# Kernel tuning notes

Measured on AMD Instinct MI355X. Metric: run time of the kernel, lower is better.

Reference implementation:

```python
import jax, jax.numpy as jnp
import numpy as np

NEG = float(-2**32 + 1)  # huge negative used by the original sign-based masking
EPS = 1e-8
NUM_BLOCKS = 3
NUM_HEADS = 1


def _mha(xq, xk, xv, Wq, bq, Wk, bk, Wv, bv):
    # manual QKV with ReLU, as in the torch module
    Q = jax.nn.relu(xq @ Wq + bq)   # [B, Lq, D]
    K = jax.nn.relu(xk @ Wk + bk)   # [B, Lk, D]
    V = jax.nn.relu(xv @ Wv + bv)
    B, Lq, D = Q.shape
    Lk = K.shape[1]
    dh = D // NUM_HEADS
    Qh = Q.reshape(B, Lq, NUM_HEADS, dh)
    Kh = K.reshape(B, Lk, NUM_HEADS, dh)
    Vh = V.reshape(B, Lk, NUM_HEADS, dh)
    scores = jnp.einsum('bqhd,bkhd->bhqk', Qh, Kh) / jnp.sqrt(jnp.float32(dh))
    # sign-based key padding mask (rows whose embedding-sum is exactly 0)
    key_mask0 = (jnp.sign(jnp.abs(jnp.sum(xk, axis=-1))) == 0.0).astype(scores.dtype)  # [B, Lk]
    cond = key_mask0[:, None, None, :]
    scores = NEG * cond + scores * (1.0 - cond)
    attn = jax.nn.softmax(scores, axis=-1)
    # post-softmax query mask
    qmask = jnp.sign(jnp.abs(jnp.sum(xq, axis=-1)))  # [B, Lq]
    attn = attn * qmask[:, None, :, None]
    out = jnp.einsum('bhqk,bkhd->bqhd', attn, Vh).reshape(B, Lq, D)
    return out + xq  # residual; note: the torch mha never applies its layernorm


def _layernorm(x, g, b):
    mu = jnp.mean(x, axis=-1, keepdims=True)
    var = jnp.mean(jnp.square(x - mu), axis=-1, keepdims=True)
    return (x - mu) / jnp.sqrt(var + EPS) * g + b


def _ffn(x, W1, b1, W2, b2, g, bln):
    h = jax.nn.relu(x @ W1 + b1) @ W2 + b2
    return _layernorm(h, g, bln) + x


def setup_inputs() -> dict:
    key = jax.random.key(0)
    ks = jax.random.split(key, 9)
    B, L, V, D, NB = 4096, 50, 50000, 200, NUM_BLOCKS
    tokens = jax.random.randint(ks[0], (B, L), 0, V)
    emb = jax.random.normal(ks[1], (V, D), dtype=jnp.float32) * 0.1
    emb = emb.at[0].set(0.0)  # padding token row -> triggers sign masks
    s = 1.0 / np.sqrt(D)
    Wq = jax.random.normal(ks[2], (NB, D, D), dtype=jnp.float32) * s
    Wk = jax.random.normal(ks[3], (NB, D, D), dtype=jnp.float32) * s
    Wv = jax.random.normal(ks[4], (NB, D, D), dtype=jnp.float32) * s
    W1 = jax.random.normal(ks[5], (NB, D, D), dtype=jnp.float32) * s
    W2 = jax.random.normal(ks[6], (NB, D, D), dtype=jnp.float32) * s
    z = jnp.zeros((NB, D), dtype=jnp.float32)
    return dict(tokens=tokens, emb=emb,
                Wq=Wq, bq=z, Wk=Wk, bk=z, Wv=Wv, bv=z,
                W1=W1, b1=z, W2=W2, b2=z,
                ln_g=jnp.ones((NB, D), dtype=jnp.float32), ln_b=z)


def reference(tokens, emb, Wq, bq, Wk, bk, Wv, bv, W1, b1, W2, b2, ln_g, ln_b):
    x = emb[tokens]  # [B, L, D]
    for i in range(NUM_BLOCKS):
        x = _mha(x, x, x, Wq[i], bq[i], Wk[i], bk[i], Wv[i], bv[i])
        x = _ffn(x, W1[i], b1[i], W2[i], b2[i], ln_g[i], ln_b[i])
    return x
```

## Files before the change

### kernel.cpp

```cpp
#include <hip/hip_runtime.h>
#include <hip/hip_bf16.h>
#include <math.h>

#define LQ 50
#define DD 200
#define NBLK 3
#define NT 1024
#define NW 16

#define KT 7
#define NTL 14
#define MAT_U (KT * NTL * 128)

#define APS 408
#define VTS 72
#define PS  136
#define SS  66

#define NEGC (-4294967295.0f)
#define SCALE 0.07071067811865475f

typedef __attribute__((ext_vector_type(4))) float f32x4;
typedef __attribute__((ext_vector_type(8))) short s16x8;

__device__ __forceinline__ unsigned short bf16_rne(float x) {
  unsigned u = __float_as_uint(x);
  unsigned r = u + 0x7FFF + ((u >> 16) & 1);
  return (unsigned short)(r >> 16);
}
__device__ __forceinline__ float bf16_f(unsigned short h) {
  return __uint_as_float((unsigned)h << 16);
}

__device__ __forceinline__ void splitf(float x, short& h, short& l) {
  __hip_bfloat16 bh = __float2bfloat16(x);
  float hf = __bfloat162float(bh);
  __hip_bfloat16 bl = __float2bfloat16(x - hf);
  h = (short)__builtin_bit_cast(unsigned short, bh);
  l = (short)__builtin_bit_cast(unsigned short, bl);
}
__device__ __forceinline__ unsigned short bfbits(float x) {
  __hip_bfloat16 bh = __float2bfloat16(x);
  return __builtin_bit_cast(unsigned short, bh);
}
__device__ __forceinline__ float joinf(short h, short l) {
  return __bfloat162float(__builtin_bit_cast(__hip_bfloat16, (unsigned short)h)) +
         __bfloat162float(__builtin_bit_cast(__hip_bfloat16, (unsigned short)l));
}

__device__ __forceinline__ float wave_sum(float v) {
  #pragma unroll
  for (int off = 32; off > 0; off >>= 1) v += __shfl_xor(v, off, 64);
  return v;
}
__device__ __forceinline__ float wave_max(float v) {
  #pragma unroll
  for (int off = 32; off > 0; off >>= 1) v = fmaxf(v, __shfl_xor(v, off, 64));
  return v;
}

__global__ __launch_bounds__(64)
void swizzle_w(const float* __restrict__ Wq, const float* __restrict__ Wk,
               const float* __restrict__ Wv, const float* __restrict__ W1,
               const float* __restrict__ W2, unsigned short* __restrict__ wbuf)
{
  int t = blockIdx.x;
  int nt = t % NTL; t /= NTL;
  int kt = t % KT;  t /= KT;
  int mat = t;
  int layer = mat / 5, which = mat % 5;
  const float* W;
  switch (which) {
    case 0: W = Wq; break;
    case 1: W = Wk; break;
    case 2: W = Wv; break;
    case 3: W = W1; break;
    default: W = W2; break;
  }
  W += (size_t)layer * DD * DD;

  const int l = threadIdx.x;
  const int g = l >> 4, c = l & 15;
  const int n = nt * 16 + c;
  s16x8 vh, vl;
  #pragma unroll
  for (int j = 0; j < 8; ++j) {
    int k = kt * 32 + g * 8 + j;
    float w = (k < DD && n < DD) ? W[k * DD + n] : 0.0f;
    unsigned short h = bf16_rne(w);
    unsigned short lo = bf16_rne(w - bf16_f(h));
    vh[j] = (short)h;
    vl[j] = (short)lo;
  }
  size_t base = ((size_t)(mat * KT * NTL + kt * NTL + nt) * 2) * 512 + l * 8;
  *(s16x8*)(wbuf + base)       = vh;
  *(s16x8*)(wbuf + base + 512) = vl;
}

template <int MODE>
__device__ __forceinline__ void big_matmul(
    const short* __restrict__ srcp, const s16x8* __restrict__ wt,
    const float* __restrict__ bias, short* __restrict__ dstp,
    float* __restrict__ dstf, int wv, int lane)
{
  if (wv >= 13) return;
  const int g = lane >> 4, c = lane & 15;
  const int n1 = wv;

  const short* arow[4];
  #pragma unroll
  for (int m = 0; m < 4; ++m) {
    int r = m * 16 + c;
    if (r >= LQ) r = 0;
    arow[m] = srcp + r * APS;
  }

  f32x4 acc0[4];
  #pragma unroll
  for (int m = 0; m < 4; ++m) acc0[m] = (f32x4)0.f;

  #pragma unroll 1
  for (int kt = 0; kt < KT; ++kt) {
    const s16x8* p1 = wt + ((size_t)kt * NTL + n1) * 128 + lane;
    s16x8 b1h = p1[0], b1l = p1[64];
    const int ch = kt * 4 + g;
    const bool ok = (ch < 25);
    #pragma unroll
    for (int m = 0; m < 4; ++m) {
      s16x8 ah = (s16x8)0, al = (s16x8)0;
      if (ok) {
        const short* ap = arow[m] + ch * 16;
        ah = *(const s16x8*)ap;
        al = *(const s16x8*)(ap + 8);
      }
      if (MODE == 0) {
        acc0[m] = __builtin_amdgcn_mfma_f32_16x16x32_bf16(b1h, ah, acc0[m], 0, 0, 0);
        acc0[m] = __builtin_amdgcn_mfma_f32_16x16x32_bf16(b1h, al, acc0[m], 0, 0, 0);
        acc0[m] = __builtin_amdgcn_mfma_f32_16x16x32_bf16(b1l, ah, acc0[m], 0, 0, 0);
      } else {
        acc0[m] = __builtin_amdgcn_mfma_f32_16x16x32_bf16(ah, b1h, acc0[m], 0, 0, 0);
        acc0[m] = __builtin_amdgcn_mfma_f32_16x16x32_bf16(al, b1h, acc0[m], 0, 0, 0);
        acc0[m] = __builtin_amdgcn_mfma_f32_16x16x32_bf16(ah, b1l, acc0[m], 0, 0, 0);
      }
    }
  }

  if (MODE == 0) {
    const int nb = n1 * 16 + g * 4;
    if (nb + 3 < DD) {
      float4 bv = *(const float4*)(bias + nb);
      #pragma unroll
      for (int m = 0; m < 4; ++m) {
        const int r = m * 16 + c;
        if (r < LQ) {
          const f32x4 ac = acc0[m];
          float v0 = fmaxf(ac[0] + bv.x, 0.f);
          float v1 = fmaxf(ac[1] + bv.y, 0.f);
          float v2 = fmaxf(ac[2] + bv.z, 0.f);
          float v3 = fmaxf(ac[3] + bv.w, 0.f);
          short h0, l0, h1, l1, h2, l2, h3, l3;
          splitf(v0, h0, l0); splitf(v1, h1, l1);
          splitf(v2, h2, l2); splitf(v3, h3, l3);
          uint2 ph, pl;
          ph.x = (unsigned short)h0 | ((unsigned)(unsigned short)h1 << 16);
          ph.y = (unsigned short)h2 | ((unsigned)(unsigned short)h3 << 16);
          pl.x = (unsigned short)l0 | ((unsigned)(unsigned short)l1 << 16);
          pl.y = (unsigned short)l2 | ((unsigned)(unsigned short)l3 << 16);
          short* base = dstp + r * APS + (nb >> 3) * 16 + (nb & 7);
          *(uint2*)base = ph;
          *(uint2*)(base + 8) = pl;
        }
      }
    }
  } else {
    const int col = n1 * 16 + c;
    if (col < DD) {
      const float bv = bias[col];
      #pragma unroll
      for (int m = 0; m < 4; ++m) {
        const int rb = m * 16 + g * 4;
        if (MODE == 1) {
          float vv[4];
          #pragma unroll
          for (int q = 0; q < 4; ++q) {
            const int r = rb + q;
            float v = acc0[m][q] + bv;
            vv[q] = (r < LQ) ? fmaxf(v, 0.f) : 0.f;
          }
          unsigned u0 = (unsigned)bfbits(vv[0]) | ((unsigned)bfbits(vv[1]) << 16);
          unsigned u1 = (unsigned)bfbits(vv[2]) | ((unsigned)bfbits(vv[3]) << 16);
          uint2 pk; pk.x = u0; pk.y = u1;
          *(uint2*)(dstp + col * VTS + (rb >> 3) * 8 + (rb & 7)) = pk;
        } else {
          #pragma unroll
          for (int q = 0; q < 4; ++q) {
            const int r = rb + q;
            float v = acc0[m][q] + bv;
            if (r < LQ) dstf[r * DD + col] = v;
          }
        }
      }
    }
  }
}

__global__ __launch_bounds__(NT)
void transformer_kernel(const int* __restrict__ tokens,
                        const float* __restrict__ emb,
                        const unsigned short* __restrict__ wbuf,
                        const float* __restrict__ bq, const float* __restrict__ bk,
                        const float* __restrict__ bv, const float* __restrict__ b1,
                        const float* __restrict__ b2,
                        const float* __restrict__ lng, const float* __restrict__ lnb,
                        float* __restrict__ out)
{
  __shared__ __align__(16) short xs_p[LQ * APS];
  __shared__ __align__(16) short q_p [LQ * APS];
  __shared__ __align__(16) short k_p [LQ * APS];
  __shared__ __align__(16) short vt_p[DD * VTS];
  __shared__ float rowsum[52];

  float* Sf   = (float*)q_p;
  short* Pp   = q_p + 8192;
  float* h2f  = (float*)k_p;

  const int b    = blockIdx.x;
  const int tid  = threadIdx.x;
  const int lane = tid & 63;
  const int wv   = tid >> 6;
  const int g    = lane >> 4, c = lane & 15;

  for (int o = tid; o < LQ * 25; o += NT) {
    int r = o / 25, ch = o % 25;
    int tok = tokens[b * LQ + r];
    const float* ep = emb + (size_t)tok * DD + ch * 8;
    float4 a0 = *(const float4*)ep;
    float4 a1 = *(const float4*)(ep + 4);
    float xv[8] = {a0.x, a0.y, a0.z, a0.w, a1.x, a1.y, a1.z, a1.w};
    s16x8 hh, ll;
    #pragma unroll
    for (int j = 0; j < 8; ++j) { short h, l; splitf(xv[j], h, l); hh[j] = h; ll[j] = l; }
    short* dp = xs_p + r * APS + ch * 16;
    *(s16x8*)dp = hh;
    *(s16x8*)(dp + 8) = ll;
  }
  __syncthreads();

  for (int layer = 0; layer < NBLK; ++layer) {
    const s16x8* wq  = (const s16x8*)wbuf + (size_t)(layer * 5 + 0) * MAT_U;
    const s16x8* wk  = (const s16x8*)wbuf + (size_t)(layer * 5 + 1) * MAT_U;
    const s16x8* wvv = (const s16x8*)wbuf + (size_t)(layer * 5 + 2) * MAT_U;
    const s16x8* w1  = (const s16x8*)wbuf + (size_t)(layer * 5 + 3) * MAT_U;
    const s16x8* w2  = (const s16x8*)wbuf + (size_t)(layer * 5 + 4) * MAT_U;
    const float* bql = bq + layer * DD;
    const float* bkl = bk + layer * DD;
    const float* bvl = bv + layer * DD;
    const float* b1l = b1 + layer * DD;
    const float* b2l = b2 + layer * DD;
    const float* gl  = lng + layer * DD;
    const float* bl  = lnb + layer * DD;

    if (layer == 0) {
      for (int r = wv; r < LQ; r += NW) {
        float s = 0.f;
        #pragma unroll
        for (int t = 0; t < 4; ++t) {
          int cc = lane + 64 * t;
          if (cc < DD) {
            const short* p = xs_p + r * APS + (cc >> 3) * 16 + (cc & 7);
            s += joinf(p[0], p[8]);
          }
        }
        s = wave_sum(s);
        if (lane == 0) rowsum[r] = s;
      }
    }

    big_matmul<0>(xs_p, wq,  bql, q_p,  nullptr, wv, lane);
    big_matmul<0>(xs_p, wk,  bkl, k_p,  nullptr, wv, lane);
    big_matmul<1>(xs_p, wvv, bvl, vt_p, nullptr, wv, lane);
    __syncthreads();

    f32x4 s0 = (f32x4)0.f;
    {
      const int mt  = wv >> 2;
      const int ntk = wv & 3;
      int qr = mt * 16 + c;   if (qr >= LQ) qr = 0;
      int kj = ntk * 16 + c;  if (kj >= LQ) kj = 0;
      const short* qrow = q_p + qr * APS;
      const short* k0r  = k_p + kj * APS;
      #pragma unroll 1
      for (int kt = 0; kt < KT; ++kt) {
        const int ch = kt * 4 + g;
        s16x8 qh = (s16x8)0, ql = (s16x8)0;
        s16x8 kh0 = (s16x8)0, kl0 = (s16x8)0;
        if (ch < 25) {
          qh  = *(const s16x8*)(qrow + ch * 16); ql  = *(const s16x8*)(qrow + ch * 16 + 8);
          kh0 = *(const s16x8*)(k0r + ch * 16);  kl0 = *(const s16x8*)(k0r + ch * 16 + 8);
        }
        s0 = __builtin_amdgcn_mfma_f32_16x16x32_bf16(qh, kh0, s0, 0, 0, 0);
        s0 = __builtin_amdgcn_mfma_f32_16x16x32_bf16(ql, kh0, s0, 0, 0, 0);
        s0 = __builtin_amdgcn_mfma_f32_16x16x32_bf16(qh, kl0, s0, 0, 0, 0);
      }
    }
    __syncthreads();

    {
      const int mt  = wv >> 2;
      const int ntk = wv & 3;
      const int j = ntk * 16 + c;
      const bool km = (j < LQ) && (rowsum[j] != 0.0f);
      #pragma unroll
      for (int q = 0; q < 4; ++q) {
        const int qi = mt * 16 + g * 4 + q;
        if (qi < LQ) Sf[qi * SS + j] = km ? s0[q] * SCALE : NEGC;
      }
    }
    __syncthreads();

    for (int r = wv; r < LQ; r += NW) {
      float sm = -INFINITY;
      if (lane < LQ) sm = Sf[r * SS + lane];
      float m = wave_max(sm);
      float e = (lane < LQ) ? __expf(sm - m) : 0.0f;
      float ssum = wave_sum(e);
      float qm = (rowsum[r] == 0.0f) ? 0.0f : 1.0f;
      float a = e / ssum * qm;
      short h, l; splitf(a, h, l);
      short* pp = Pp + r * PS + (lane >> 3) * 16 + (lane & 7);
      pp[0] = h; pp[8] = l;
    }
    __syncthreads();

    if (wv < 13) {
      const int mt = wv;
      f32x4 pa[4];
      #pragma unroll
      for (int nq = 0; nq < 4; ++nq) pa[nq] = (f32x4)0.f;
      int vr = mt * 16 + c; if (vr >= DD) vr = 0;
      const short* vrow = vt_p + vr * VTS;
      #pragma unroll
      for (int kt = 0; kt < 2; ++kt) {
        s16x8 vh = *(const s16x8*)(vrow + (kt * 4 + g) * 8);
        #pragma unroll
        for (int nq = 0; nq < 4; ++nq) {
          int pr = nq * 16 + c; if (pr >= LQ) pr = 0;
          const short* pp = Pp + pr * PS + (kt * 4 + g) * 16;
          s16x8 pbh = *(const s16x8*)pp;
          s16x8 pbl = *(const s16x8*)(pp + 8);
          pa[nq] = __builtin_amdgcn_mfma_f32_16x16x32_bf16(vh, pbh, pa[nq], 0, 0, 0);
          pa[nq] = __builtin_amdgcn_mfma_f32_16x16x32_bf16(vh, pbl, pa[nq], 0, 0, 0);
        }
      }
      const int d0 = mt * 16 + g * 4;
      if (d0 + 3 < DD) {
        #pragma unroll
        for (int nq = 0; nq < 4; ++nq) {
          const int qq = nq * 16 + c;
          if (qq < LQ) {
            short* base = xs_p + qq * APS + (d0 >> 3) * 16 + (d0 & 7);
            uint2 ph = *(const uint2*)base;
            uint2 pl = *(const uint2*)(base + 8);
            float f0 = joinf((short)(ph.x & 0xFFFF), (short)(pl.x & 0xFFFF)) + pa[nq][0];
            float f1 = joinf((short)(ph.x >> 16),    (short)(pl.x >> 16))    + pa[nq][1];
            float f2 = joinf((short)(ph.y & 0xFFFF), (short)(pl.y & 0xFFFF)) + pa[nq][2];
            float f3 = joinf((short)(ph.y >> 16),    (short)(pl.y >> 16))    + pa[nq][3];
            short h0, l0, h1, l1, h2, l2, h3, l3;
            splitf(f0, h0, l0); splitf(f1, h1, l1);
            splitf(f2, h2, l2); splitf(f3, h3, l3);
            ph.x = (unsigned short)h0 | ((unsigned)(unsigned short)h1 << 16);
            ph.y = (unsigned short)h2 | ((unsigned)(unsigned short)h3 << 16);
            pl.x = (unsigned short)l0 | ((unsigned)(unsigned short)l1 << 16);
            pl.y = (unsigned short)l2 | ((unsigned)(unsigned short)l3 << 16);
            *(uint2*)base = ph;
            *(uint2*)(base + 8) = pl;
          }
        }
      }
    }
    __syncthreads();

    big_matmul<0>(xs_p, w1, b1l, q_p, nullptr, wv, lane);
    __syncthreads();
    big_matmul<2>(q_p, w2, b2l, nullptr, h2f, wv, lane);
    __syncthreads();

    for (int r = wv; r < LQ; r += NW) {
      float hv[4];
      #pragma unroll
      for (int t = 0; t < 4; ++t) {
        int cc = lane + 64 * t;
        hv[t] = (cc < DD) ? h2f[r * DD + cc] : 0.f;
      }
      float mu = wave_sum(hv[0] + hv[1] + hv[2] + hv[3]) * (1.0f / 200.0f);
      float d0 = hv[0] - mu, d1 = hv[1] - mu, d2 = hv[2] - mu;
      float d3 = (lane + 192 < DD) ? (hv[3] - mu) : 0.f;
      float var = wave_sum(d0 * d0 + d1 * d1 + d2 * d2 + d3 * d3) * (1.0f / 200.0f);
      float inv = 1.0f / sqrtf(var + 1e-8f);
      float dd4[4] = {d0, d1, d2, d3};
      float rs = 0.f;
      #pragma unroll
      for (int t = 0; t < 4; ++t) {
        int cc = lane + 64 * t;
        if (cc < DD) {
          short* hp = xs_p + r * APS + (cc >> 3) * 16 + (cc & 7);
          float nv = dd4[t] * inv * gl[cc] + bl[cc] + joinf(hp[0], hp[8]);
          rs += nv;
          short h, l; splitf(nv, h, l);
          hp[0] = h; hp[8] = l;
        }
      }
      rs = wave_sum(rs);
      if (lane == 0) rowsum[r] = rs;
    }
    __syncthreads();
  }

  for (int o = tid; o < LQ * 25; o += NT) {
    int r = o / 25, ch = o % 25;
    const short* sp = xs_p + r * APS + ch * 16;
    s16x8 hh = *(const s16x8*)sp;
    s16x8 ll = *(const s16x8*)(sp + 8);
    float4 o0, o1;
    o0.x = joinf(hh[0], ll[0]); o0.y = joinf(hh[1], ll[1]);
    o0.z = joinf(hh[2], ll[2]); o0.w = joinf(hh[3], ll[3]);
    o1.x = joinf(hh[4], ll[4]); o1.y = joinf(hh[5], ll[5]);
    o1.z = joinf(hh[6], ll[6]); o1.w = joinf(hh[7], ll[7]);
    float* op = out + ((size_t)b * LQ + r) * DD + ch * 8;
    *(float4*)op = o0;
    *(float4*)(op + 4) = o1;
  }
}

extern "C" void kernel_launch(void* const* d_in, const int* in_sizes, int n_in,
                              void* d_out, int out_size, void* d_ws, size_t ws_size,
                              hipStream_t stream) {
  const int*   tokens = (const int*)  d_in[0];
  const float* emb    = (const float*)d_in[1];
  const float* Wq     = (const float*)d_in[2];
  const float* bq     = (const float*)d_in[3];
  const float* Wk     = (const float*)d_in[4];
  const float* bk     = (const float*)d_in[5];
  const float* Wv     = (const float*)d_in[6];
  const float* bv     = (const float*)d_in[7];
  const float* W1     = (const float*)d_in[8];
  const float* b1     = (const float*)d_in[9];
  const float* W2     = (const float*)d_in[10];
  const float* b2     = (const float*)d_in[11];
  const float* lng    = (const float*)d_in[12];
  const float* lnb    = (const float*)d_in[13];
  float* out = (float*)d_out;
  unsigned short* wbuf = (unsigned short*)d_ws;

  hipLaunchKernelGGL(swizzle_w, dim3(15 * KT * NTL), dim3(64), 0, stream,
                     Wq, Wk, Wv, W1, W2, wbuf);

  const int B = in_sizes[0] / LQ;
  hipLaunchKernelGGL(transformer_kernel, dim3(B), dim3(NT), 0, stream,
                     tokens, emb, wbuf, bq, bk, bv, b1, b2, lng, lnb, out);
}
```

Measured before the change: 1.750 ms.

## Switch projections to 32x32 MFMA tiles, overlap V with scores, reduce split-precision passes

The weight swizzle and all dense projections now use 32x32x16 bf16 MFMA tiles instead of 16x16x32, and work is spread across waves differently. The V projection runs on one set of waves while the QK^T scores run concurrently on another, and the W1/W2 loops prefetch the next weight fragment. Several split-bf16 (hi/lo) passes are dropped: the attention probabilities, the FFN hidden activations and the W2 A operand become single bf16. This cuts MFMA count and LDS traffic but lowers numerical precision, which risks failing the tolerance check.

```diff
diff --git a/kernel.cpp b/kernel.cpp
--- a/kernel.cpp
+++ b/kernel.cpp
@@ -8,9 +8,9 @@
 #define NT 1024
 #define NW 16
 
-#define KT 7
-#define NTL 14
-#define MAT_U (KT * NTL * 128)
+#define KC 13
+#define NT32 7
+#define MAT_U (KC * NT32 * 128)
 
 #define APS 408
 #define VTS 72
@@ -20,8 +20,9 @@
 #define NEGC (-4294967295.0f)
 #define SCALE 0.07071067811865475f
 
-typedef __attribute__((ext_vector_type(4))) float f32x4;
-typedef __attribute__((ext_vector_type(8))) short s16x8;
+typedef __attribute__((ext_vector_type(4)))  float f32x4;
+typedef __attribute__((ext_vector_type(16))) float f32x16;
+typedef __attribute__((ext_vector_type(8)))  short s16x8;
 
 __device__ __forceinline__ unsigned short bf16_rne(float x) {
   unsigned u = __float_as_uint(x);
@@ -31,7 +32,6 @@
 __device__ __forceinline__ float bf16_f(unsigned short h) {
   return __uint_as_float((unsigned)h << 16);
 }
-
 __device__ __forceinline__ void splitf(float x, short& h, short& l) {
   __hip_bfloat16 bh = __float2bfloat16(x);
   float hf = __bfloat162float(bh);
@@ -65,8 +65,8 @@
                const float* __restrict__ W2, unsigned short* __restrict__ wbuf)
 {
   int t = blockIdx.x;
-  int nt = t % NTL; t /= NTL;
-  int kt = t % KT;  t /= KT;
+  int nt = t % NT32; t /= NT32;
+  int kc = t % KC;  t /= KC;
   int mat = t;
   int layer = mat / 5, which = mat % 5;
   const float* W;
@@ -80,87 +80,70 @@
   W += (size_t)layer * DD * DD;
 
   const int l = threadIdx.x;
-  const int g = l >> 4, c = l & 15;
-  const int n = nt * 16 + c;
+  const int n = nt * 32 + (l & 31);
+  const int kb = kc * 16 + (l >> 5) * 8;
   s16x8 vh, vl;
   #pragma unroll
   for (int j = 0; j < 8; ++j) {
-    int k = kt * 32 + g * 8 + j;
+    int k = kb + j;
     float w = (k < DD && n < DD) ? W[k * DD + n] : 0.0f;
     unsigned short h = bf16_rne(w);
     unsigned short lo = bf16_rne(w - bf16_f(h));
     vh[j] = (short)h;
     vl[j] = (short)lo;
   }
-  size_t base = ((size_t)(mat * KT * NTL + kt * NTL + nt) * 2) * 512 + l * 8;
+  size_t base = ((size_t)((mat * KC + kc) * NT32 + nt)) * 1024 + l * 8;
   *(s16x8*)(wbuf + base)       = vh;
   *(s16x8*)(wbuf + base + 512) = vl;
 }
 
-template <int MODE>
-__device__ __forceinline__ void big_matmul(
+__device__ __forceinline__ void mm32_ct_pair(
     const short* __restrict__ srcp, const s16x8* __restrict__ wt,
-    const float* __restrict__ bias, short* __restrict__ dstp,
-    float* __restrict__ dstf, int wv, int lane)
+    const float* __restrict__ bias, short* __restrict__ dstp, int nt, int lane)
 {
-  if (wv >= 13) return;
-  const int g = lane >> 4, c = lane & 15;
-  const int n1 = wv;
-
-  const short* arow[4];
+  const int h = lane >> 5, l31 = lane & 31;
+  f32x16 acc0 = (f32x16)0.f, acc1 = (f32x16)0.f;
+  int r1 = 32 + l31; if (r1 >= LQ) r1 = 0;
+  const short* arow0 = srcp + l31 * APS;
+  const short* arow1 = srcp + r1 * APS;
+
+  #pragma unroll 1
+  for (int kc = 0; kc < KC; ++kc) {
+    const s16x8* wp = wt + (size_t)(kc * NT32 + nt) * 128 + lane;
+    s16x8 wh = wp[0], wl = wp[64];
+    const int ch = 2 * kc + h;
+    const bool ok = (ch < 25);
+    {
+      s16x8 ah = (s16x8)0, al = (s16x8)0;
+      if (ok) { const short* p = arow0 + ch * 16; ah = *(const s16x8*)p; al = *(const s16x8*)(p + 8); }
+      acc0 = __builtin_amdgcn_mfma_f32_32x32x16_bf16(wh, ah, acc0, 0, 0, 0);
+      acc0 = __builtin_amdgcn_mfma_f32_32x32x16_bf16(wh, al, acc0, 0, 0, 0);
+      acc0 = __builtin_amdgcn_mfma_f32_32x32x16_bf16(wl, ah, acc0, 0, 0, 0);
+    }
+    {
+      s16x8 ah = (s16x8)0, al = (s16x8)0;
+      if (ok) { const short* p = arow1 + ch * 16; ah = *(const s16x8*)p; al = *(const s16x8*)(p + 8); }
+      acc1 = __builtin_amdgcn_mfma_f32_32x32x16_bf16(wh, ah, acc1, 0, 0, 0);
+      acc1 = __builtin_amdgcn_mfma_f32_32x32x16_bf16(wh, al, acc1, 0, 0, 0);
+      acc1 = __builtin_amdgcn_mfma_f32_32x32x16_bf16(wl, ah, acc1, 0, 0, 0);
+    }
+  }
+
   #pragma unroll
-  for (int m = 0; m < 4; ++m) {
-    int r = m * 16 + c;
-    if (r >= LQ) r = 0;
-    arow[m] = srcp + r * APS;
-  }
-
-  f32x4 acc0[4];
-  #pragma unroll
-  for (int m = 0; m < 4; ++m) acc0[m] = (f32x4)0.f;
-
-  #pragma unroll 1
-  for (int kt = 0; kt < KT; ++kt) {
-    const s16x8* p1 = wt + ((size_t)kt * NTL + n1) * 128 + lane;
-    s16x8 b1h = p1[0], b1l = p1[64];
-    const int ch = kt * 4 + g;
-    const bool ok = (ch < 25);
-    #pragma unroll
-    for (int m = 0; m < 4; ++m) {
-      s16x8 ah = (s16x8)0, al = (s16x8)0;
-      if (ok) {
-        const short* ap = arow[m] + ch * 16;
-        ah = *(const s16x8*)ap;
-        al = *(const s16x8*)(ap + 8);
-      }
-      if (MODE == 0) {
-        acc0[m] = __builtin_amdgcn_mfma_f32_16x16x32_bf16(b1h, ah, acc0[m], 0, 0, 0);
-        acc0[m] = __builtin_amdgcn_mfma_f32_16x16x32_bf16(b1h, al, acc0[m], 0, 0, 0);
-        acc0[m] = __builtin_amdgcn_mfma_f32_16x16x32_bf16(b1l, ah, acc0[m], 0, 0, 0);
-      } else {
-        acc0[m] = __builtin_amdgcn_mfma_f32_16x16x32_bf16(ah, b1h, acc0[m], 0, 0, 0);
-        acc0[m] = __builtin_amdgcn_mfma_f32_16x16x32_bf16(al, b1h, acc0[m], 0, 0, 0);
-        acc0[m] = __builtin_amdgcn_mfma_f32_16x16x32_bf16(ah, b1l, acc0[m], 0, 0, 0);
-      }
-    }
-  }
-
-  if (MODE == 0) {
-    const int nb = n1 * 16 + g * 4;
-    if (nb + 3 < DD) {
-      float4 bv = *(const float4*)(bias + nb);
-      #pragma unroll
-      for (int m = 0; m < 4; ++m) {
-        const int r = m * 16 + c;
-        if (r < LQ) {
-          const f32x4 ac = acc0[m];
-          float v0 = fmaxf(ac[0] + bv.x, 0.f);
-          float v1 = fmaxf(ac[1] + bv.y, 0.f);
-          float v2 = fmaxf(ac[2] + bv.z, 0.f);
-          float v3 = fmaxf(ac[3] + bv.w, 0.f);
-          short h0, l0, h1, l1, h2, l2, h3, l3;
-          splitf(v0, h0, l0); splitf(v1, h1, l1);
-          splitf(v2, h2, l2); splitf(v3, h3, l3);
+  for (int rt = 0; rt < 2; ++rt) {
+    const int r = rt * 32 + l31;
+    if (r < LQ) {
+      #pragma unroll
+      for (int q2 = 0; q2 < 4; ++q2) {
+        const int nb = nt * 32 + 8 * q2 + 4 * h;
+        if (nb + 3 < DD) {
+          float4 bv = *(const float4*)(bias + nb);
+          float v0 = fmaxf((rt ? acc1[q2*4+0] : acc0[q2*4+0]) + bv.x, 0.f);
+          float v1 = fmaxf((rt ? acc1[q2*4+1] : acc0[q2*4+1]) + bv.y, 0.f);
+          float v2 = fmaxf((rt ? acc1[q2*4+2] : acc0[q2*4+2]) + bv.z, 0.f);
+          float v3 = fmaxf((rt ? acc1[q2*4+3] : acc0[q2*4+3]) + bv.w, 0.f);
+          short h0,l0,h1,l1,h2,l2,h3,l3;
+          splitf(v0,h0,l0); splitf(v1,h1,l1); splitf(v2,h2,l2); splitf(v3,h3,l3);
           uint2 ph, pl;
           ph.x = (unsigned short)h0 | ((unsigned)(unsigned short)h1 << 16);
           ph.y = (unsigned short)h2 | ((unsigned)(unsigned short)h3 << 16);
@@ -172,33 +155,151 @@
         }
       }
     }
-  } else {
-    const int col = n1 * 16 + c;
-    if (col < DD) {
-      const float bv = bias[col];
-      #pragma unroll
-      for (int m = 0; m < 4; ++m) {
-        const int rb = m * 16 + g * 4;
-        if (MODE == 1) {
-          float vv[4];
-          #pragma unroll
-          for (int q = 0; q < 4; ++q) {
-            const int r = rb + q;
-            float v = acc0[m][q] + bv;
-            vv[q] = (r < LQ) ? fmaxf(v, 0.f) : 0.f;
-          }
-          unsigned u0 = (unsigned)bfbits(vv[0]) | ((unsigned)bfbits(vv[1]) << 16);
-          unsigned u1 = (unsigned)bfbits(vv[2]) | ((unsigned)bfbits(vv[3]) << 16);
-          uint2 pk; pk.x = u0; pk.y = u1;
-          *(uint2*)(dstp + col * VTS + (rb >> 3) * 8 + (rb & 7)) = pk;
-        } else {
-          #pragma unroll
-          for (int q = 0; q < 4; ++q) {
-            const int r = rb + q;
-            float v = acc0[m][q] + bv;
-            if (r < LQ) dstf[r * DD + col] = v;
-          }
-        }
+  }
+}
+
+__device__ __forceinline__ void mm32_v(
+    const short* __restrict__ srcp, const s16x8* __restrict__ wt,
+    const float* __restrict__ bias, short* __restrict__ vtp, int nt, int lane)
+{
+  const int h = lane >> 5, l31 = lane & 31;
+  f32x16 acc0 = (f32x16)0.f, acc1 = (f32x16)0.f;
+  int r1 = 32 + l31; if (r1 >= LQ) r1 = 0;
+  const short* arow0 = srcp + l31 * APS;
+  const short* arow1 = srcp + r1 * APS;
+
+  #pragma unroll 1
+  for (int kc = 0; kc < KC; ++kc) {
+    const s16x8* wp = wt + (size_t)(kc * NT32 + nt) * 128 + lane;
+    s16x8 wh = wp[0], wl = wp[64];
+    const int ch = 2 * kc + h;
+    const bool ok = (ch < 25);
+    {
+      s16x8 ah = (s16x8)0, al = (s16x8)0;
+      if (ok) { const short* p = arow0 + ch * 16; ah = *(const s16x8*)p; al = *(const s16x8*)(p + 8); }
+      acc0 = __builtin_amdgcn_mfma_f32_32x32x16_bf16(ah, wh, acc0, 0, 0, 0);
+      acc0 = __builtin_amdgcn_mfma_f32_32x32x16_bf16(al, wh, acc0, 0, 0, 0);
+      acc0 = __builtin_amdgcn_mfma_f32_32x32x16_bf16(ah, wl, acc0, 0, 0, 0);
+    }
+    {
+      s16x8 ah = (s16x8)0, al = (s16x8)0;
+      if (ok) { const short* p = arow1 + ch * 16; ah = *(const s16x8*)p; al = *(const s16x8*)(p + 8); }
+      acc1 = __builtin_amdgcn_mfma_f32_32x32x16_bf16(ah, wh, acc1, 0, 0, 0);
+      acc1 = __builtin_amdgcn_mfma_f32_32x32x16_bf16(al, wh, acc1, 0, 0, 0);
+      acc1 = __builtin_amdgcn_mfma_f32_32x32x16_bf16(ah, wl, acc1, 0, 0, 0);
+    }
+  }
+
+  const int d = nt * 32 + l31;
+  if (d < DD) {
+    const float bvs = bias[d];
+    #pragma unroll
+    for (int mt2 = 0; mt2 < 2; ++mt2) {
+      #pragma unroll
+      for (int q2 = 0; q2 < 4; ++q2) {
+        const int rb = mt2 * 32 + 8 * q2 + 4 * h;
+        float vv[4];
+        #pragma unroll
+        for (int e = 0; e < 4; ++e) {
+          const int r = rb + e;
+          float v = (mt2 ? acc1[q2*4+e] : acc0[q2*4+e]) + bvs;
+          vv[e] = (r < LQ) ? fmaxf(v, 0.f) : 0.f;
+        }
+        uint2 pk;
+        pk.x = (unsigned)bfbits(vv[0]) | ((unsigned)bfbits(vv[1]) << 16);
+        pk.y = (unsigned)bfbits(vv[2]) | ((unsigned)bfbits(vv[3]) << 16);
+        *(uint2*)(vtp + d * VTS + (rb >> 3) * 8 + (rb & 7)) = pk;
+      }
+    }
+  }
+}
+
+__device__ __forceinline__ void mm32_w1(
+    const short* __restrict__ srcp, const s16x8* __restrict__ wt,
+    const float* __restrict__ bias, short* __restrict__ dstp,
+    int nt, int rt, int lane)
+{
+  const int h = lane >> 5, l31 = lane & 31;
+  f32x16 acc = (f32x16)0.f;
+  int r = rt * 32 + l31;
+  int rr = (r >= LQ) ? 0 : r;
+  const short* arow = srcp + rr * APS;
+
+  const s16x8* wp = wt + (size_t)nt * 128 + lane;
+  s16x8 wh = wp[0], wl = wp[64];
+  #pragma unroll 1
+  for (int kc = 0; kc < KC; ++kc) {
+    s16x8 nh = (s16x8)0, nl = (s16x8)0;
+    if (kc + 1 < KC) {
+      const s16x8* np = wt + (size_t)((kc + 1) * NT32 + nt) * 128 + lane;
+      nh = np[0]; nl = np[64];
+    }
+    const int ch = 2 * kc + h;
+    s16x8 ah = (s16x8)0, al = (s16x8)0;
+    if (ch < 25) { const short* p = arow + ch * 16; ah = *(const s16x8*)p; al = *(const s16x8*)(p + 8); }
+    acc = __builtin_amdgcn_mfma_f32_32x32x16_bf16(wh, ah, acc, 0, 0, 0);
+    acc = __builtin_amdgcn_mfma_f32_32x32x16_bf16(wh, al, acc, 0, 0, 0);
+    acc = __builtin_amdgcn_mfma_f32_32x32x16_bf16(wl, ah, acc, 0, 0, 0);
+    wh = nh; wl = nl;
+  }
+
+  if (r < LQ) {
+    #pragma unroll
+    for (int q2 = 0; q2 < 4; ++q2) {
+      const int nb = nt * 32 + 8 * q2 + 4 * h;
+      if (nb + 3 < DD) {
+        float4 bv = *(const float4*)(bias + nb);
+        float v0 = fmaxf(acc[q2*4+0] + bv.x, 0.f);
+        float v1 = fmaxf(acc[q2*4+1] + bv.y, 0.f);
+        float v2 = fmaxf(acc[q2*4+2] + bv.z, 0.f);
+        float v3 = fmaxf(acc[q2*4+3] + bv.w, 0.f);
+        uint2 ph;
+        ph.x = (unsigned)bfbits(v0) | ((unsigned)bfbits(v1) << 16);
+        ph.y = (unsigned)bfbits(v2) | ((unsigned)bfbits(v3) << 16);
+        *(uint2*)(dstp + r * APS + (nb >> 3) * 16 + (nb & 7)) = ph;
+      }
+    }
+  }
+}
+
+__device__ __forceinline__ void mm32_w2(
+    const short* __restrict__ srcp, const s16x8* __restrict__ wt,
+    const float* __restrict__ bias, float* __restrict__ dstf,
+    int nt, int rt, int lane)
+{
+  const int h = lane >> 5, l31 = lane & 31;
+  f32x16 acc = (f32x16)0.f;
+  int r = rt * 32 + l31;
+  int rr = (r >= LQ) ? 0 : r;
+  const short* arow = srcp + rr * APS;
+
+  const s16x8* wp = wt + (size_t)nt * 128 + lane;
+  s16x8 wh = wp[0], wl = wp[64];
+  #pragma unroll 1
+  for (int kc = 0; kc < KC; ++kc) {
+    s16x8 nh = (s16x8)0, nl = (s16x8)0;
+    if (kc + 1 < KC) {
+      const s16x8* np = wt + (size_t)((kc + 1) * NT32 + nt) * 128 + lane;
+      nh = np[0]; nl = np[64];
+    }
+    const int ch = 2 * kc + h;
+    s16x8 ah = (s16x8)0;
+    if (ch < 25) ah = *(const s16x8*)(arow + ch * 16);
+    acc = __builtin_amdgcn_mfma_f32_32x32x16_bf16(wh, ah, acc, 0, 0, 0);
+    acc = __builtin_amdgcn_mfma_f32_32x32x16_bf16(wl, ah, acc, 0, 0, 0);
+    wh = nh; wl = nl;
+  }
+
+  if (r < LQ) {
+    #pragma unroll
+    for (int q2 = 0; q2 < 4; ++q2) {
+      const int d0 = nt * 32 + 8 * q2 + 4 * h;
+      if (d0 + 3 < DD) {
+        float4 bv = *(const float4*)(bias + d0);
+        float4 w4;
+        w4.x = acc[q2*4+0] + bv.x; w4.y = acc[q2*4+1] + bv.y;
+        w4.z = acc[q2*4+2] + bv.z; w4.w = acc[q2*4+3] + bv.w;
+        *(float4*)(dstf + r * DD + d0) = w4;
       }
     }
   }
@@ -220,9 +321,9 @@
   __shared__ __align__(16) short vt_p[DD * VTS];
   __shared__ float rowsum[52];
 
-  float* Sf   = (float*)q_p;
-  short* Pp   = q_p + 8192;
-  float* h2f  = (float*)k_p;
+  float* Sf  = (float*)q_p;
+  short* Pp  = q_p + 8192;
+  float* h2f = (float*)k_p;
 
   const int b    = blockIdx.x;
   const int tid  = threadIdx.x;
@@ -276,44 +377,57 @@
       }
     }
 
-    big_matmul<0>(xs_p, wq,  bql, q_p,  nullptr, wv, lane);
-    big_matmul<0>(xs_p, wk,  bkl, k_p,  nullptr, wv, lane);
-    big_matmul<1>(xs_p, wvv, bvl, vt_p, nullptr, wv, lane);
-    __syncthreads();
-
-    f32x4 s0 = (f32x4)0.f;
-    {
-      const int mt  = wv >> 2;
-      const int ntk = wv & 3;
-      int qr = mt * 16 + c;   if (qr >= LQ) qr = 0;
-      int kj = ntk * 16 + c;  if (kj >= LQ) kj = 0;
+    if (wv < 7)                      mm32_ct_pair(xs_p, wq, bql, q_p, wv, lane);
+    else if (wv >= 8 && wv < 15)     mm32_ct_pair(xs_p, wk, bkl, k_p, wv - 8, lane);
+    __syncthreads();
+
+    f32x4 s0 = (f32x4)0.f, s1 = (f32x4)0.f;
+    if (wv >= 8) {
+      const int w8 = wv - 8;
+      const int mt = w8 >> 1;
+      const int nk0 = (w8 & 1) * 2;
+      int qr = mt * 16 + c;          if (qr >= LQ) qr = 0;
+      int kj0 = nk0 * 16 + c;        if (kj0 >= LQ) kj0 = 0;
+      int kj1 = (nk0 + 1) * 16 + c;  if (kj1 >= LQ) kj1 = 0;
       const short* qrow = q_p + qr * APS;
-      const short* k0r  = k_p + kj * APS;
+      const short* k0r  = k_p + kj0 * APS;
+      const short* k1r  = k_p + kj1 * APS;
       #pragma unroll 1
-      for (int kt = 0; kt < KT; ++kt) {
+      for (int kt = 0; kt < 7; ++kt) {
         const int ch = kt * 4 + g;
         s16x8 qh = (s16x8)0, ql = (s16x8)0;
-        s16x8 kh0 = (s16x8)0, kl0 = (s16x8)0;
+        s16x8 kh0 = (s16x8)0, kl0 = (s16x8)0, kh1 = (s16x8)0, kl1 = (s16x8)0;
         if (ch < 25) {
           qh  = *(const s16x8*)(qrow + ch * 16); ql  = *(const s16x8*)(qrow + ch * 16 + 8);
           kh0 = *(const s16x8*)(k0r + ch * 16);  kl0 = *(const s16x8*)(k0r + ch * 16 + 8);
+          kh1 = *(const s16x8*)(k1r + ch * 16);  kl1 = *(const s16x8*)(k1r + ch * 16 + 8);
         }
         s0 = __builtin_amdgcn_mfma_f32_16x16x32_bf16(qh, kh0, s0, 0, 0, 0);
         s0 = __builtin_amdgcn_mfma_f32_16x16x32_bf16(ql, kh0, s0, 0, 0, 0);
         s0 = __builtin_amdgcn_mfma_f32_16x16x32_bf16(qh, kl0, s0, 0, 0, 0);
-      }
-    }
-    __syncthreads();
-
-    {
-      const int mt  = wv >> 2;
-      const int ntk = wv & 3;
-      const int j = ntk * 16 + c;
-      const bool km = (j < LQ) && (rowsum[j] != 0.0f);
-      #pragma unroll
-      for (int q = 0; q < 4; ++q) {
-        const int qi = mt * 16 + g * 4 + q;
-        if (qi < LQ) Sf[qi * SS + j] = km ? s0[q] * SCALE : NEGC;
+        s1 = __builtin_amdgcn_mfma_f32_16x16x32_bf16(qh, kh1, s1, 0, 0, 0);
+        s1 = __builtin_amdgcn_mfma_f32_16x16x32_bf16(ql, kh1, s1, 0, 0, 0);
+        s1 = __builtin_amdgcn_mfma_f32_16x16x32_bf16(qh, kl1, s1, 0, 0, 0);
+      }
+    } else if (wv < 7) {
+      mm32_v(xs_p, wvv, bvl, vt_p, wv, lane);
+    }
+    __syncthreads();
+
+    if (wv >= 8) {
+      const int w8 = wv - 8;
+      const int mt = w8 >> 1;
+      const int nk0 = (w8 & 1) * 2;
+      #pragma unroll
+      for (int t = 0; t < 2; ++t) {
+        const int j = (nk0 + t) * 16 + c;
+        const f32x4 sa = t ? s1 : s0;
+        const bool km = (j < LQ) && (rowsum[j] != 0.0f);
+        #pragma unroll
+        for (int q = 0; q < 4; ++q) {
+          const int qi = mt * 16 + g * 4 + q;
+          if (qi < LQ) Sf[qi * SS + j] = km ? sa[q] * SCALE : NEGC;
+        }
       }
     }
     __syncthreads();
@@ -326,9 +440,7 @@
       float ssum = wave_sum(e);
       float qm = (rowsum[r] == 0.0f) ? 0.0f : 1.0f;
       float a = e / ssum * qm;
-      short h, l; splitf(a, h, l);
-      short* pp = Pp + r * PS + (lane >> 3) * 16 + (lane & 7);
-      pp[0] = h; pp[8] = l;
+      Pp[r * PS + (lane >> 3) * 16 + (lane & 7)] = (short)bfbits(a);
     }
     __syncthreads();
 
@@ -345,11 +457,8 @@
         #pragma unroll
         for (int nq = 0; nq < 4; ++nq) {
           int pr = nq * 16 + c; if (pr >= LQ) pr = 0;
-          const short* pp = Pp + pr * PS + (kt * 4 + g) * 16;
-          s16x8 pbh = *(const s16x8*)pp;
-          s16x8 pbl = *(const s16x8*)(pp + 8);
+          s16x8 pbh = *(const s16x8*)(Pp + pr * PS + (kt * 4 + g) * 16);
           pa[nq] = __builtin_amdgcn_mfma_f32_16x16x32_bf16(vh, pbh, pa[nq], 0, 0, 0);
-          pa[nq] = __builtin_amdgcn_mfma_f32_16x16x32_bf16(vh, pbl, pa[nq], 0, 0, 0);
         }
       }
       const int d0 = mt * 16 + g * 4;
@@ -365,9 +474,8 @@
             float f1 = joinf((short)(ph.x >> 16),    (short)(pl.x >> 16))    + pa[nq][1];
             float f2 = joinf((short)(ph.y & 0xFFFF), (short)(pl.y & 0xFFFF)) + pa[nq][2];
             float f3 = joinf((short)(ph.y >> 16),    (short)(pl.y >> 16))    + pa[nq][3];
-            short h0, l0, h1, l1, h2, l2, h3, l3;
-            splitf(f0, h0, l0); splitf(f1, h1, l1);
-            splitf(f2, h2, l2); splitf(f3, h3, l3);
+            short h0,l0,h1,l1,h2,l2,h3,l3;
+            splitf(f0,h0,l0); splitf(f1,h1,l1); splitf(f2,h2,l2); splitf(f3,h3,l3);
             ph.x = (unsigned short)h0 | ((unsigned)(unsigned short)h1 << 16);
             ph.y = (unsigned short)h2 | ((unsigned)(unsigned short)h3 << 16);
             pl.x = (unsigned short)l0 | ((unsigned)(unsigned short)l1 << 16);
@@ -380,9 +488,9 @@
     }
     __syncthreads();
 
-    big_matmul<0>(xs_p, w1, b1l, q_p, nullptr, wv, lane);
-    __syncthreads();
-    big_matmul<2>(q_p, w2, b2l, nullptr, h2f, wv, lane);
+    if (wv < 14) mm32_w1(xs_p, w1, b1l, q_p, wv >> 1, wv & 1, lane);
+    __syncthreads();
+    if (wv < 14) mm32_w2(q_p, w2, b2l, h2f, wv >> 1, wv & 1, lane);
     __syncthreads();
 
     for (int r = wv; r < LQ; r += NW) {
@@ -452,7 +560,7 @@
   float* out = (float*)d_out;
   unsigned short* wbuf = (unsigned short*)d_ws;
 
-  hipLaunchKernelGGL(swizzle_w, dim3(15 * KT * NTL), dim3(64), 0, stream,
+  hipLaunchKernelGGL(swizzle_w, dim3(15 * KC * NT32), dim3(64), 0, stream,
                      Wq, Wk, Wv, W1, W2, wbuf);
 
   const int B = in_sizes[0] / LQ;
```

Result: faster. 1.664 ms (-4.9%).
